# Kernel optimization log

Hardware: AMD Instinct MI355X
Metric: run time of the kernel (lower is better)

Reference implementation:

```python
import jax, jax.numpy as jnp
import numpy as np

B, T, D = 1, 2048, 1024
E, DFF = 8, 4096


def setup_inputs() -> dict:
    key = jax.random.key(0)
    k1, k2, k3, k4 = jax.random.split(key, 4)
    x = jax.random.normal(k1, (B, T, D), dtype=jnp.float32)
    Wg = jax.random.normal(k2, (D, E), dtype=jnp.float32) * (1.0 / np.sqrt(D))
    w1 = jax.random.normal(k3, (D, DFF), dtype=jnp.float32) * (1.0 / np.sqrt(D))
    w2 = jax.random.normal(k4, (DFF, D), dtype=jnp.float32) * (1.0 / np.sqrt(DFF))
    return {"x": x, "Wg": Wg, "w1": w1, "w2": w2}


def _gating(logits):
    # logits: [S, E]; capacity = S (per source code)
    S, num_e = logits.shape
    gates = jax.nn.softmax(logits.astype(jnp.float32), axis=1)  # [S,E] fp32
    idx1 = jnp.argmax(gates, axis=1)                            # top-1 expert
    mask1 = jax.nn.one_hot(idx1, num_e, dtype=jnp.int32)        # [S,E]
    logits_ex1 = jnp.where(mask1.astype(bool), -jnp.inf, logits)
    idx2 = jnp.argmax(logits_ex1, axis=1)                       # top-2 expert
    mask2 = jax.nn.one_hot(idx2, num_e, dtype=jnp.int32)
    # slot position of each token inside its expert buffer
    loc1 = jnp.cumsum(mask1, axis=0) - 1                        # [S,E]
    loc2 = jnp.cumsum(mask2, axis=0) - 1 + jnp.sum(mask1, axis=0, keepdims=True)
    loc1_s = jnp.sum(loc1 * mask1, axis=1)                      # [S] int
    loc2_s = jnp.sum(loc2 * mask2, axis=1)
    g1 = jnp.sum(gates * mask1, axis=1)                         # [S]
    g2 = jnp.sum(gates * mask2, axis=1)
    denom = jnp.maximum(g1 + g2, jnp.finfo(jnp.float32).eps)
    g1, g2 = g1 / denom, g2 / denom
    cap = S
    loc1_sc = jax.nn.one_hot(loc1_s, cap, dtype=jnp.float32)    # [S,C]
    loc2_sc = jax.nn.one_hot(loc2_s, cap, dtype=jnp.float32)
    # combine_weights: [S,E,C]
    combine = (g1[:, None] * mask1)[:, :, None] * loc1_sc[:, None, :] \
            + (g2[:, None] * mask2)[:, :, None] * loc2_sc[:, None, :]
    dispatch_mask = combine != 0
    return combine.astype(logits.dtype), dispatch_mask


def reference(x, Wg, w1, w2):
    d_model = x.shape[2]
    xs = x.reshape(-1, d_model)                                  # [S,D]
    logits = xs @ Wg                                             # gate linear
    combine, dispatch_mask = _gating(logits)
    # one-hot scatter dispatch: [S,E,C] x [S,D] -> [E,C,D]
    dispatched = jnp.einsum('sec,sm->ecm', dispatch_mask.astype(jnp.float32), xs)
    # all-to-all is an identity permutation of the expert dim in single-process ref
    expert_out = jax.nn.relu(dispatched @ w1) @ w2               # [E,C,D]
    # one-hot gather combine: [S,E,C] x [E,C,D] -> [S,D]
    out = jnp.einsum('sec,ecm->sm', combine, expert_out)
    return out.reshape(x.shape)
```

## Files before the change

### kernel.cpp

```cpp
#include <hip/hip_runtime.h>
#include <stdint.h>


typedef __attribute__((ext_vector_type(4))) float f32x4;
typedef __attribute__((ext_vector_type(16))) float f32x16;
typedef __attribute__((ext_vector_type(8))) short bf16x8;
typedef __attribute__((ext_vector_type(4))) ushort u16x4;

#define GPTR(p) (const __attribute__((address_space(1))) void*)(p)
#define LPTR(p) (__attribute__((address_space(3))) void*)(p)

__device__ __forceinline__ ushort f2bf(float f) {
  uint32_t u = __float_as_uint(f);
  uint32_t r = (u + 0x7FFFu + ((u >> 16) & 1u)) >> 16;
  return (ushort)r;
}
__device__ __forceinline__ float bf2f(ushort u) {
  return __uint_as_float((uint32_t)u << 16);
}

__global__ __launch_bounds__(256) void prep(const float* __restrict__ x,
                                            const float* __restrict__ w1,
                                            const float* __restrict__ w2,
                                            ushort* __restrict__ xb,
                                            ushort* __restrict__ w1t,
                                            ushort* __restrict__ w2t) {
  const int b = blockIdx.x, tid = threadIdx.x;
  if (b < 2048) {
    int i = b * 256 + tid;
    f32x4 v = __builtin_nontemporal_load(&((const f32x4*)x)[i]);
    u16x4 o;
    o.x = f2bf(v.x); o.y = f2bf(v.y); o.z = f2bf(v.z); o.w = f2bf(v.w);
    ((u16x4*)xb)[i] = o;
    return;
  }
  const float* in;
  ushort* outp;
  int R, C, bt;
  if (b < 3072) { bt = b - 2048; in = w1; outp = w1t; R = 1024; C = 4096; }
  else          { bt = b - 3072; in = w2; outp = w2t; R = 4096; C = 1024; }
  const int ntx = C / 64;
  const int bx = bt % ntx, by = bt / ntx;
  const int c0 = bx * 64, r0 = by * 64;
  __shared__ float tile[64][65];
  const int tx = tid & 15, ty = tid >> 4;
#pragma unroll
  for (int rr = 0; rr < 64; rr += 16) {
    f32x4 v = __builtin_nontemporal_load(
        (const f32x4*)&in[(size_t)(r0 + ty + rr) * C + c0 + tx * 4]);
    tile[ty + rr][tx * 4 + 0] = v.x;
    tile[ty + rr][tx * 4 + 1] = v.y;
    tile[ty + rr][tx * 4 + 2] = v.z;
    tile[ty + rr][tx * 4 + 3] = v.w;
  }
  __syncthreads();
#pragma unroll
  for (int cc = 0; cc < 64; cc += 16) {
    const int c = ty + cc;
    const int r = tx * 4;
    u16x4 o;
    o.x = f2bf(tile[r + 0][c]);
    o.y = f2bf(tile[r + 1][c]);
    o.z = f2bf(tile[r + 2][c]);
    o.w = f2bf(tile[r + 3][c]);
    *(u16x4*)&outp[(size_t)(c0 + c) * R + r0 + r] = o;
  }
}

__global__ void reduce_out(float* __restrict__ out, const ushort* __restrict__ pb,
                           int SD) {
  int i = blockIdx.x * blockDim.x + threadIdx.x;
  if (i >= SD / 4) return;
  f32x4 a = __builtin_nontemporal_load(&((const f32x4*)out)[i]);
#pragma unroll
  for (int j = 0; j < 3; ++j) {
    u16x4 u = __builtin_nontemporal_load(&((const u16x4*)(pb + (size_t)j * SD))[i]);
    a[0] += bf2f(u.x); a[1] += bf2f(u.y); a[2] += bf2f(u.z); a[3] += bf2f(u.w);
  }
  __builtin_nontemporal_store(a, &((f32x4*)out)[i]);
}

template <int MODE>
__global__ __launch_bounds__(512) void gemm_pipe(const ushort* __restrict__ A,
                                                 const ushort* __restrict__ Bt,
                                                 void* __restrict__ C0,
                                                 void* __restrict__ C1,
                                                 int M, int N, int Ks, int Ktot,
                                                 int ncx, int cpz) {
  constexpr int BM = 128, BN = 256, BK = 64;
  __shared__ ushort As[3][BM * BK];
  __shared__ ushort Bs[3][BN * BK];

  const int tid = threadIdx.x;
  const int lane = tid & 63, wid = tid >> 6;
  const int wr = wid >> 2, wc = wid & 3;

  const int ck = blockIdx.x & 7;
  const int w = blockIdx.x >> 3;
  const int bz = ck / cpz;
  const int rem = ck % cpz;
  const int bx = (rem % ncx) * 4 + (w & 3);
  const int by = (rem / ncx) * 8 + (w >> 2);
  const int row0 = by * BM, col0 = bx * BN;
  const int kbase = bz * Ks;

  f32x16 acc[2][2];
#pragma unroll
  for (int m = 0; m < 2; ++m)
#pragma unroll
    for (int n = 0; n < 2; ++n) acc[m][n] = (f32x16)(0.f);

  const int rA = tid >> 3;
  const int cb = (tid & 7) * 16;
  auto stage_part = [&](int buf, int k0, int p) {
    if (p == 0) {
#pragma unroll
      for (int i = 0; i < 2; ++i) {
        int r = i * 64 + rA;
        int csw = cb ^ ((r & 7) << 4);
        __builtin_amdgcn_global_load_lds(
            GPTR((const char*)(A + (size_t)(row0 + r) * Ktot + k0) + csw),
            LPTR((char*)&As[buf][0] + i * 8192 + wid * 1024), 16, 0, 0);
      }
    } else {
#pragma unroll
      for (int j2 = 0; j2 < 2; ++j2) {
        int j = (p - 1) * 2 + j2;
        int r = j * 64 + rA;
        int csw = cb ^ ((r & 7) << 4);
        __builtin_amdgcn_global_load_lds(
            GPTR((const char*)(Bt + (size_t)(col0 + r) * Ktot + k0) + csw),
            LPTR((char*)&Bs[buf][0] + j * 8192 + wid * 1024), 16, 0, 0);
      }
    }
  };
  auto stage = [&](int buf, int k0) {
    stage_part(buf, k0, 0); stage_part(buf, k0, 1); stage_part(buf, k0, 2);
  };

  const int nt = Ks / BK;
  stage(0, kbase);
  stage(1, kbase + BK);

  for (int t = 0; t < nt; ++t) {
    if (t < nt - 1) asm volatile("s_waitcnt vmcnt(6)" ::: "memory");
    else            asm volatile("s_waitcnt vmcnt(0)" ::: "memory");
    __builtin_amdgcn_sched_barrier(0);
    __builtin_amdgcn_s_barrier();
    __builtin_amdgcn_sched_barrier(0);

    const ushort* Ab = As[t % 3];
    const ushort* Bb = Bs[t % 3];
    const bool pf = (t + 2 < nt);
    const int knext = kbase + (t + 2) * BK;
    const int pbuf = (t + 2) % 3;

    bf16x8 a[2][2], b[2][2];
    auto read_slice = [&](int s, int sb) {
      const int kb2 = s * 32 + (lane >> 5) * 16;
#pragma unroll
      for (int m = 0; m < 2; ++m) {
        int R = wr * 64 + m * 32 + (lane & 31);
        a[sb][m] = *(const bf16x8*)((const char*)Ab + R * 128 + (kb2 ^ ((R & 7) << 4)));
      }
#pragma unroll
      for (int n = 0; n < 2; ++n) {
        int R = wc * 64 + n * 32 + (lane & 31);
        b[sb][n] = *(const bf16x8*)((const char*)Bb + R * 128 + (kb2 ^ ((R & 7) << 4)));
      }
    };

    read_slice(0, 0);
#pragma unroll
    for (int s = 0; s < 4; ++s) {
      if (s < 3) read_slice(s + 1, (s + 1) & 1);
      if (s < 3 && pf) stage_part(pbuf, knext, s);
      __builtin_amdgcn_s_setprio(1);
#pragma unroll
      for (int m = 0; m < 2; ++m)
#pragma unroll
        for (int n = 0; n < 2; ++n)
          acc[m][n] = __builtin_amdgcn_mfma_f32_32x32x16_bf16(a[s & 1][m], b[s & 1][n],
                                                              acc[m][n], 0, 0, 0);
      __builtin_amdgcn_s_setprio(0);
    }
  }

  const int rbase = row0 + wr * 64, cbase = col0 + wc * 64;
#pragma unroll
  for (int m = 0; m < 2; ++m) {
#pragma unroll
    for (int n = 0; n < 2; ++n) {
      const int col = cbase + n * 32 + (lane & 31);
#pragma unroll
      for (int r = 0; r < 16; ++r) {
        const int row = rbase + m * 32 + (r & 3) + 8 * (r >> 2) + 4 * (lane >> 5);
        float v = acc[m][n][r];
        size_t idx = (size_t)row * N + col;
        if (MODE == 1) {
          v = v > 0.f ? v : 0.f;
          __builtin_nontemporal_store(f2bf(v), &((ushort*)C0)[idx]);
        } else {
          if (bz == 0)
            __builtin_nontemporal_store(v, &((float*)C0)[idx]);
          else
            __builtin_nontemporal_store(f2bf(v),
                &((ushort*)C1)[(size_t)(bz - 1) * M * N + idx]);
        }
      }
    }
  }
}

extern "C" void kernel_launch(void* const* d_in, const int* in_sizes, int n_in,
                              void* d_out, int out_size, void* d_ws, size_t ws_size,
                              hipStream_t stream) {
  const float* x  = (const float*)d_in[0];
  const float* w1 = (const float*)d_in[2];
  const float* w2 = (const float*)d_in[3];
  float* out = (float*)d_out;

  constexpr int S = 2048, D = 1024, F = 4096;
  char* ws = (char*)d_ws;
  ushort* xb  = (ushort*)(ws);
  ushort* w1t = (ushort*)(ws + (size_t)S * D * 2);
  ushort* w2t = (ushort*)(ws + (size_t)(S * D + F * D) * 2);
  ushort* H   = (ushort*)(ws + (size_t)(S * D + 2 * F * D) * 2);
  ushort* pb = (ushort*)(ws);

  hipLaunchKernelGGL(prep, dim3(4096), dim3(256), 0, stream,
                     x, w1, w2, xb, w1t, w2t);
  hipLaunchKernelGGL((gemm_pipe<1>), dim3(256), dim3(512), 0, stream,
                     xb, w1t, (void*)H, nullptr, S, F, D, D, 4, 8);
  hipLaunchKernelGGL((gemm_pipe<2>), dim3(256), dim3(512), 0, stream,
                     H, w2t, (void*)out, (void*)pb, S, D, F / 4, F, 1, 2);
  hipLaunchKernelGGL(reduce_out, dim3((S * D / 4 + 255) / 256), dim3(256), 0, stream,
                     out, pb, S * D);
}
```

Baseline: 77.26 us.

## Drop nontemporal hints and setprio; write all split-K partials as bf16

Replaces all nontemporal loads and stores in the prep, reduce and GEMM kernels with plain memory accesses. Removes the s_setprio raise around the MFMA blocks. When the workspace is large enough, every split-K partial of the second GEMM, including the first, goes to a separate bf16 buffer, and the reduce kernel sums four parts from zero instead of reading an fp32 partial from the output. This trades cache-policy and scheduling hints for ordinary caching, and storing the first partial in bf16 loses some precision.

```diff
diff --git a/kernel.cpp b/kernel.cpp
--- a/kernel.cpp
+++ b/kernel.cpp
@@ -28,7 +28,7 @@
   const int b = blockIdx.x, tid = threadIdx.x;
   if (b < 2048) {
     int i = b * 256 + tid;
-    f32x4 v = __builtin_nontemporal_load(&((const f32x4*)x)[i]);
+    f32x4 v = ((const f32x4*)x)[i];
     u16x4 o;
     o.x = f2bf(v.x); o.y = f2bf(v.y); o.z = f2bf(v.z); o.w = f2bf(v.w);
     ((u16x4*)xb)[i] = o;
@@ -46,8 +46,7 @@
   const int tx = tid & 15, ty = tid >> 4;
 #pragma unroll
   for (int rr = 0; rr < 64; rr += 16) {
-    f32x4 v = __builtin_nontemporal_load(
-        (const f32x4*)&in[(size_t)(r0 + ty + rr) * C + c0 + tx * 4]);
+    f32x4 v = *(const f32x4*)&in[(size_t)(r0 + ty + rr) * C + c0 + tx * 4];
     tile[ty + rr][tx * 4 + 0] = v.x;
     tile[ty + rr][tx * 4 + 1] = v.y;
     tile[ty + rr][tx * 4 + 2] = v.z;
@@ -68,25 +67,26 @@
 }
 
 __global__ void reduce_out(float* __restrict__ out, const ushort* __restrict__ pb,
-                           int SD) {
+                           int SD, int nparts) {
   int i = blockIdx.x * blockDim.x + threadIdx.x;
   if (i >= SD / 4) return;
-  f32x4 a = __builtin_nontemporal_load(&((const f32x4*)out)[i]);
-#pragma unroll
-  for (int j = 0; j < 3; ++j) {
-    u16x4 u = __builtin_nontemporal_load(&((const u16x4*)(pb + (size_t)j * SD))[i]);
+  f32x4 a;
+  if (nparts == 4) a = (f32x4){0.f, 0.f, 0.f, 0.f};
+  else             a = ((const f32x4*)out)[i];
+  for (int j = 0; j < nparts; ++j) {
+    u16x4 u = ((const u16x4*)(pb + (size_t)j * SD))[i];
     a[0] += bf2f(u.x); a[1] += bf2f(u.y); a[2] += bf2f(u.z); a[3] += bf2f(u.w);
   }
-  __builtin_nontemporal_store(a, &((f32x4*)out)[i]);
+  ((f32x4*)out)[i] = a;
 }
 
 template <int MODE>
 __global__ __launch_bounds__(512) void gemm_pipe(const ushort* __restrict__ A,
                                                  const ushort* __restrict__ Bt,
                                                  void* __restrict__ C0,
-                                                 void* __restrict__ C1,
+                                                 ushort* __restrict__ C1,
                                                  int M, int N, int Ks, int Ktot,
-                                                 int ncx, int cpz) {
+                                                 int ncx, int cpz, int z0p) {
   constexpr int BM = 128, BN = 256, BK = 64;
   __shared__ ushort As[3][BM * BK];
   __shared__ ushort Bs[3][BN * BK];
@@ -175,14 +175,12 @@
     for (int s = 0; s < 4; ++s) {
       if (s < 3) read_slice(s + 1, (s + 1) & 1);
       if (s < 3 && pf) stage_part(pbuf, knext, s);
-      __builtin_amdgcn_s_setprio(1);
 #pragma unroll
       for (int m = 0; m < 2; ++m)
 #pragma unroll
         for (int n = 0; n < 2; ++n)
           acc[m][n] = __builtin_amdgcn_mfma_f32_32x32x16_bf16(a[s & 1][m], b[s & 1][n],
                                                               acc[m][n], 0, 0, 0);
-      __builtin_amdgcn_s_setprio(0);
     }
   }
 
@@ -199,13 +197,14 @@
         size_t idx = (size_t)row * N + col;
         if (MODE == 1) {
           v = v > 0.f ? v : 0.f;
-          __builtin_nontemporal_store(f2bf(v), &((ushort*)C0)[idx]);
+          ((ushort*)C0)[idx] = f2bf(v);
         } else {
-          if (bz == 0)
-            __builtin_nontemporal_store(v, &((float*)C0)[idx]);
+          if (z0p)
+            C1[(size_t)bz * M * N + idx] = f2bf(v);
+          else if (bz == 0)
+            ((float*)C0)[idx] = v;
           else
-            __builtin_nontemporal_store(f2bf(v),
-                &((ushort*)C1)[(size_t)(bz - 1) * M * N + idx]);
+            C1[(size_t)(bz - 1) * M * N + idx] = f2bf(v);
         }
       }
     }
@@ -226,14 +225,19 @@
   ushort* w1t = (ushort*)(ws + (size_t)S * D * 2);
   ushort* w2t = (ushort*)(ws + (size_t)(S * D + F * D) * 2);
   ushort* H   = (ushort*)(ws + (size_t)(S * D + 2 * F * D) * 2);
-  ushort* pb = (ushort*)(ws);
+
+  const size_t hi_off = (size_t)(S * D + 2 * F * D + S * F) * 2;
+  const bool big = ws_size >= hi_off + (size_t)4 * S * D * 2;
+  ushort* pb = big ? (ushort*)(ws + hi_off) : (ushort*)(ws);
+  const int z0p = big ? 1 : 0;
+  const int nparts = big ? 4 : 3;
 
   hipLaunchKernelGGL(prep, dim3(4096), dim3(256), 0, stream,
                      x, w1, w2, xb, w1t, w2t);
   hipLaunchKernelGGL((gemm_pipe<1>), dim3(256), dim3(512), 0, stream,
-                     xb, w1t, (void*)H, nullptr, S, F, D, D, 4, 8);
+                     xb, w1t, (void*)H, (ushort*)nullptr, S, F, D, D, 4, 8, 0);
   hipLaunchKernelGGL((gemm_pipe<2>), dim3(256), dim3(512), 0, stream,
-                     H, w2t, (void*)out, (void*)pb, S, D, F / 4, F, 1, 2);
+                     H, w2t, (void*)out, pb, S, D, F / 4, F, 1, 2, z0p);
   hipLaunchKernelGGL(reduce_out, dim3((S * D / 4 + 255) / 256), dim3(256), 0, stream,
-                     out, pb, S * D);
-}
+                     out, pb, S * D, nparts);
+}
```

Result: faster. 68.76 us (-11.0%).
